# Kernel optimization log

Measured on AMD Instinct MI355X. Metric: run time of the kernel, lower is better.

## Reference

```python
import jax, jax.numpy as jnp
import numpy as np

FEAT = 2048
NUM_CLASSES = 751
EPS = 1e-5


def setup_inputs() -> dict:
    key = jax.random.key(0)
    k1, k2, k3 = jax.random.split(key, 3)
    probe_x = jax.random.normal(k1, (64, FEAT), dtype=jnp.float32)
    gallery_x = jax.random.normal(k2, (256, FEAT), dtype=jnp.float32)
    # BatchNorm1d affine params (PyTorch init: gamma=1, beta=0)
    bn_gamma = jnp.ones((FEAT,), dtype=jnp.float32)
    bn_beta = jnp.zeros((FEAT,), dtype=jnp.float32)
    # classifier: weight ~ N(0, 0.001), bias = 0
    W = jax.random.normal(k3, (NUM_CLASSES, FEAT), dtype=jnp.float32) * 0.001
    b = jnp.zeros((NUM_CLASSES,), dtype=jnp.float32)
    return {"probe_x": probe_x, "gallery_x": gallery_x,
            "bn_gamma": bn_gamma, "bn_beta": bn_beta, "W": W, "b": b}


def reference(probe_x, gallery_x, bn_gamma, bn_beta, W, b):
    n_probe, feat = probe_x.shape
    n_gallery = gallery_x.shape[0]
    # broadcast squared difference: [Np, Ng, F]
    diff = jnp.square(probe_x[:, None, :] - gallery_x[None, :, :])
    d = diff.reshape(n_probe * n_gallery, feat)
    # BatchNorm1d in training mode: biased batch statistics over the batch dim
    mean = jnp.mean(d, axis=0)
    var = jnp.mean(jnp.square(d - mean), axis=0)
    bn = (d - mean) * (bn_gamma / jnp.sqrt(var + EPS)) + bn_beta
    # Linear classifier
    cls = jnp.einsum('nf,cf->nc', bn, W) + b
    return cls.reshape(n_probe, n_gallery, -1)
```

## Files before the change

### kernel.cpp

```cpp
#include <hip/hip_runtime.h>
#include <hip/hip_bf16.h>
#include <hip/hip_fp16.h>

#define FEAT 2048
#define NCLS 751
#define NPAD 768
#define NPRB 64
#define NGAL 256
#define WSCALE 256.0f

typedef _Float16 f16x8 __attribute__((ext_vector_type(8)));
typedef float f32x4 __attribute__((ext_vector_type(4)));

__device__ __forceinline__ unsigned short f2h_u(float x) {
  union { _Float16 h; unsigned short u; } v;
  v.h = (_Float16)x;
  return v.u;
}

__global__ void stats_kernel(const float* __restrict__ P, const float* __restrict__ G,
                             const float* __restrict__ gamma, const float* __restrict__ beta,
                             float* __restrict__ st) {
  int fx = threadIdx.x & 31, ry = threadIdx.x >> 5;
  int f = blockIdx.x * 32 + fx;
  float a1 = 0, a2 = 0, a3 = 0, a4 = 0;
  for (int r = ry; r < NPRB; r += 8) {
    float x = P[r * FEAT + f], x2 = x * x;
    a1 += x; a2 += x2; a3 += x2 * x; a4 += x2 * x2;
  }
  float b1 = 0, b2 = 0, b3 = 0, b4 = 0;
  for (int r = ry; r < NGAL; r += 8) {
    float x = G[r * FEAT + f], x2 = x * x;
    b1 += x; b2 += x2; b3 += x2 * x; b4 += x2 * x2;
  }
  __shared__ float red[8][8][32];
  float vals[8] = {a1, a2, a3, a4, b1, b2, b3, b4};
#pragma unroll
  for (int m = 0; m < 8; ++m) red[m][ry][fx] = vals[m];
  __syncthreads();
  if (ry == 0) {
    float mm[8];
#pragma unroll
    for (int m = 0; m < 8; ++m) {
      float sum = 0.f;
#pragma unroll
      for (int r = 0; r < 8; ++r) sum += red[m][r][fx];
      mm[m] = sum;
    }
    float M1p = mm[0] * (1.f / NPRB), M2p = mm[1] * (1.f / NPRB);
    float M3p = mm[2] * (1.f / NPRB), M4p = mm[3] * (1.f / NPRB);
    float M1g = mm[4] * (1.f / NGAL), M2g = mm[5] * (1.f / NGAL);
    float M3g = mm[6] * (1.f / NGAL), M4g = mm[7] * (1.f / NGAL);
    float mean = M2p - 2.f * M1p * M1g + M2g;
    float Ed2 = M4p - 4.f * M3p * M1g + 6.f * M2p * M2g - 4.f * M1p * M3g + M4g;
    float var = Ed2 - mean * mean;
    float sv = gamma[f] / sqrtf(var + 1e-5f);
    st[f] = sv;
    st[FEAT + f] = beta[f] - mean * sv;
  }
}

__global__ void prepw_kernel(const float* __restrict__ W, const float* __restrict__ b,
                             const float* __restrict__ st,
                             unsigned short* __restrict__ Wp, float* __restrict__ bp) {
  int c = blockIdx.x;
  int f = threadIdx.x * 8;
  float4 w0 = make_float4(0.f, 0.f, 0.f, 0.f), w1 = w0;
  if (c < NCLS) {
    const float4* wsrc = (const float4*)(W + (size_t)c * FEAT + f);
    w0 = wsrc[0]; w1 = wsrc[1];
  }
  const float4* s4 = (const float4*)(st + f);
  float4 s0 = s4[0], s1 = s4[1];
  const float4* t4 = (const float4*)(st + FEAT + f);
  float4 t0 = t4[0], t1 = t4[1];
  uint4 u;
  u.x = (unsigned int)f2h_u(w0.x * s0.x * WSCALE) | ((unsigned int)f2h_u(w0.y * s0.y * WSCALE) << 16);
  u.y = (unsigned int)f2h_u(w0.z * s0.z * WSCALE) | ((unsigned int)f2h_u(w0.w * s0.w * WSCALE) << 16);
  u.z = (unsigned int)f2h_u(w1.x * s1.x * WSCALE) | ((unsigned int)f2h_u(w1.y * s1.y * WSCALE) << 16);
  u.w = (unsigned int)f2h_u(w1.z * s1.z * WSCALE) | ((unsigned int)f2h_u(w1.w * s1.w * WSCALE) << 16);
  *(uint4*)(Wp + (size_t)c * FEAT + f) = u;
  float acc = t0.x * w0.x + t0.y * w0.y + t0.z * w0.z + t0.w * w0.w +
              t1.x * w1.x + t1.y * w1.y + t1.z * w1.z + t1.w * w1.w;
#pragma unroll
  for (int off = 32; off > 0; off >>= 1) acc += __shfl_down(acc, off, 64);
  __shared__ float r[4];
  int wave = threadIdx.x >> 6, lane = threadIdx.x & 63;
  if (lane == 0) r[wave] = acc;
  __syncthreads();
  if (threadIdx.x == 0) bp[c] = (c < NCLS ? b[c] : 0.f) + r[0] + r[1] + r[2] + r[3];
}

__global__ void agen_kernel(const float* __restrict__ P, const float* __restrict__ G,
                            unsigned short* __restrict__ A) {
  int n = blockIdx.x;
  int p = n >> 8, g = n & 255;
  int f = threadIdx.x * 8;
  const float4* p4 = (const float4*)(P + (size_t)p * FEAT + f);
  const float4* g4 = (const float4*)(G + (size_t)g * FEAT + f);
  float4 pa = p4[0], pb = p4[1];
  float4 ga = g4[0], gb = g4[1];
  float d0 = pa.x - ga.x, d1 = pa.y - ga.y, d2 = pa.z - ga.z, d3 = pa.w - ga.w;
  float d4 = pb.x - gb.x, d5 = pb.y - gb.y, d6 = pb.z - gb.z, d7 = pb.w - gb.w;
  uint4 u;
  u.x = (unsigned int)f2h_u(d0 * d0) | ((unsigned int)f2h_u(d1 * d1) << 16);
  u.y = (unsigned int)f2h_u(d2 * d2) | ((unsigned int)f2h_u(d3 * d3) << 16);
  u.z = (unsigned int)f2h_u(d4 * d4) | ((unsigned int)f2h_u(d5 * d5) << 16);
  u.w = (unsigned int)f2h_u(d6 * d6) | ((unsigned int)f2h_u(d7 * d7) << 16);
  *(uint4*)(A + (size_t)n * FEAT + f) = u;
}

__global__ __launch_bounds__(256, 3)
void gemm_mat_kernel(const unsigned short* __restrict__ A,
                     const unsigned short* __restrict__ Wp,
                     const float* __restrict__ bp, float* __restrict__ out) {
  __shared__ unsigned short As[128 * 64];
  __shared__ unsigned short Bs[128 * 64];

  const int tid = threadIdx.x;
  const int lane = tid & 63, wave = tid >> 6;
  const int mtile = blockIdx.x, ntile = blockIdx.y;

  const int srow = tid >> 3;
  const int sch = (tid & 7) ^ (srow & 7);
  const unsigned short* ag = A + (size_t)(mtile * 128 + srow) * FEAT + sch * 8;
  const unsigned short* bg = Wp + (size_t)(ntile * 128 + srow) * FEAT + sch * 8;
  char* alds = (char*)As + wave * 1024;
  char* blds = (char*)Bs + wave * 1024;

  f32x4 acc[4][4];
#pragma unroll
  for (int mi = 0; mi < 4; ++mi)
#pragma unroll
    for (int ni = 0; ni < 4; ++ni) acc[mi][ni] = (f32x4){0.f, 0.f, 0.f, 0.f};

  const int wm = (wave & 1) * 64, wn = (wave >> 1) * 64;
  const int frow = lane & 15, fsw = lane & 7, fk = lane >> 4;

  for (int k0 = 0; k0 < FEAT; k0 += 64) {
    __syncthreads();
#pragma unroll
    for (int j = 0; j < 4; ++j) {
      __builtin_amdgcn_global_load_lds(
          (const __attribute__((address_space(1))) void*)(ag + k0 + (size_t)j * 32 * FEAT),
          (__attribute__((address_space(3))) void*)(alds + j * 4096), 16, 0, 0);
      __builtin_amdgcn_global_load_lds(
          (const __attribute__((address_space(1))) void*)(bg + k0 + (size_t)j * 32 * FEAT),
          (__attribute__((address_space(3))) void*)(blds + j * 4096), 16, 0, 0);
    }
    __syncthreads();

#pragma unroll
    for (int kk = 0; kk < 2; ++kk) {
      const int slot = (kk * 4 + fk) ^ fsw;
      f16x8 af[4], bf[4];
#pragma unroll
      for (int mi = 0; mi < 4; ++mi)
        af[mi] = *(const f16x8*)(As + (wm + mi * 16 + frow) * 64 + slot * 8);
#pragma unroll
      for (int ni = 0; ni < 4; ++ni)
        bf[ni] = *(const f16x8*)(Bs + (wn + ni * 16 + frow) * 64 + slot * 8);
#pragma unroll
      for (int mi = 0; mi < 4; ++mi)
#pragma unroll
        for (int ni = 0; ni < 4; ++ni)
          acc[mi][ni] = __builtin_amdgcn_mfma_f32_16x16x32_f16(af[mi], bf[ni], acc[mi][ni], 0, 0, 0);
    }
  }

  const int col0 = ntile * 128 + wn + (lane & 15);
  const int row0 = mtile * 128 + wm + ((lane >> 4) << 2);
#pragma unroll
  for (int ni = 0; ni < 4; ++ni) {
    int col = col0 + ni * 16;
    if (col >= NCLS) continue;
    float bv = bp[col];
#pragma unroll
    for (int mi = 0; mi < 4; ++mi) {
      int row = row0 + mi * 16;
#pragma unroll
      for (int r = 0; r < 4; ++r)
        out[(size_t)(row + r) * NCLS + col] = acc[mi][ni][r] * (1.0f / WSCALE) + bv;
    }
  }
}

extern "C" void kernel_launch(void* const* d_in, const int* in_sizes, int n_in,
                              void* d_out, int out_size, void* d_ws, size_t ws_size,
                              hipStream_t stream) {
  const float* P = (const float*)d_in[0];
  const float* G = (const float*)d_in[1];
  const float* gamma = (const float*)d_in[2];
  const float* beta = (const float*)d_in[3];
  const float* W = (const float*)d_in[4];
  const float* b = (const float*)d_in[5];
  float* out = (float*)d_out;

  float* st = (float*)d_ws;
  float* bp = st + 2 * FEAT;
  unsigned short* Wp = (unsigned short*)(bp + NPAD);
  unsigned short* A = Wp + (size_t)NPAD * FEAT;

  hipLaunchKernelGGL(agen_kernel, dim3(NPRB * NGAL), dim3(256), 0, stream, P, G, A);
  hipLaunchKernelGGL(stats_kernel, dim3(64), dim3(256), 0, stream, P, G, gamma, beta, st);
  hipLaunchKernelGGL(prepw_kernel, dim3(NPAD), dim3(256), 0, stream, W, b, st, Wp, bp);
  hipLaunchKernelGGL(gemm_mat_kernel, dim3(128, 6), dim3(256), 0, stream, A, Wp, bp, out);
}
```

Before: 166.8 us.

## Pre-swizzle weights into MFMA fragment layout and load B directly to registers

The weight-prep kernel now writes the scaled fp16 weights in a fragment-ordered layout, so each GEMM lane can read its B operand straight from global memory into registers with one coalesced vector load. This removes the B shared-memory tile and its LDS reads, and the B loads for the next k-step are double-buffered in registers while the current one computes. The cost is more registers, which could affect occupancy under launch_bounds(256,3). The prep kernel also drops from 768 blocks to 48 blocks, each looping over the whole feature dimension.

```diff
diff --git a/kernel.cpp b/kernel.cpp
--- a/kernel.cpp
+++ b/kernel.cpp
@@ -62,33 +62,45 @@
 
 __global__ void prepw_kernel(const float* __restrict__ W, const float* __restrict__ b,
                              const float* __restrict__ st,
-                             unsigned short* __restrict__ Wp, float* __restrict__ bp) {
-  int c = blockIdx.x;
-  int f = threadIdx.x * 8;
-  float4 w0 = make_float4(0.f, 0.f, 0.f, 0.f), w1 = w0;
-  if (c < NCLS) {
-    const float4* wsrc = (const float4*)(W + (size_t)c * FEAT + f);
-    w0 = wsrc[0]; w1 = wsrc[1];
-  }
-  const float4* s4 = (const float4*)(st + f);
-  float4 s0 = s4[0], s1 = s4[1];
-  const float4* t4 = (const float4*)(st + FEAT + f);
-  float4 t0 = t4[0], t1 = t4[1];
-  uint4 u;
-  u.x = (unsigned int)f2h_u(w0.x * s0.x * WSCALE) | ((unsigned int)f2h_u(w0.y * s0.y * WSCALE) << 16);
-  u.y = (unsigned int)f2h_u(w0.z * s0.z * WSCALE) | ((unsigned int)f2h_u(w0.w * s0.w * WSCALE) << 16);
-  u.z = (unsigned int)f2h_u(w1.x * s1.x * WSCALE) | ((unsigned int)f2h_u(w1.y * s1.y * WSCALE) << 16);
-  u.w = (unsigned int)f2h_u(w1.z * s1.z * WSCALE) | ((unsigned int)f2h_u(w1.w * s1.w * WSCALE) << 16);
-  *(uint4*)(Wp + (size_t)c * FEAT + f) = u;
-  float acc = t0.x * w0.x + t0.y * w0.y + t0.z * w0.z + t0.w * w0.w +
-              t1.x * w1.x + t1.y * w1.y + t1.z * w1.z + t1.w * w1.w;
-#pragma unroll
-  for (int off = 32; off > 0; off >>= 1) acc += __shfl_down(acc, off, 64);
-  __shared__ float r[4];
-  int wave = threadIdx.x >> 6, lane = threadIdx.x & 63;
-  if (lane == 0) r[wave] = acc;
+                             unsigned short* __restrict__ Wf, float* __restrict__ bp) {
+  const int nblk = blockIdx.x;
+  const int t = threadIdx.x;
+  const int row = t & 15;
+  const int c = nblk * 16 + row;
+  const int kcb = t >> 4;
+  unsigned short* wbase = Wf + (size_t)nblk * 32768;
+  float part = 0.f;
+#pragma unroll 4
+  for (int i = 0; i < 16; ++i) {
+    int kc = i * 16 + kcb;
+    int f = kc * 8;
+    float4 w0 = make_float4(0.f, 0.f, 0.f, 0.f), w1 = w0;
+    if (c < NCLS) {
+      const float4* ws = (const float4*)(W + (size_t)c * FEAT + f);
+      w0 = ws[0]; w1 = ws[1];
+    }
+    const float4* s4 = (const float4*)(st + f);
+    float4 s0 = s4[0], s1 = s4[1];
+    const float4* t4 = (const float4*)(st + FEAT + f);
+    float4 t0 = t4[0], t1 = t4[1];
+    uint4 u;
+    u.x = (unsigned int)f2h_u(w0.x * s0.x * WSCALE) | ((unsigned int)f2h_u(w0.y * s0.y * WSCALE) << 16);
+    u.y = (unsigned int)f2h_u(w0.z * s0.z * WSCALE) | ((unsigned int)f2h_u(w0.w * s0.w * WSCALE) << 16);
+    u.z = (unsigned int)f2h_u(w1.x * s1.x * WSCALE) | ((unsigned int)f2h_u(w1.y * s1.y * WSCALE) << 16);
+    u.w = (unsigned int)f2h_u(w1.z * s1.z * WSCALE) | ((unsigned int)f2h_u(w1.w * s1.w * WSCALE) << 16);
+    *(uint4*)(wbase + (size_t)kc * 128 + row * 8) = u;
+    part += t0.x * w0.x + t0.y * w0.y + t0.z * w0.z + t0.w * w0.w +
+            t1.x * w1.x + t1.y * w1.y + t1.z * w1.z + t1.w * w1.w;
+  }
+  __shared__ float red[16][16];
+  red[kcb][row] = part;
   __syncthreads();
-  if (threadIdx.x == 0) bp[c] = (c < NCLS ? b[c] : 0.f) + r[0] + r[1] + r[2] + r[3];
+  if (t < 16) {
+    float sum = (nblk * 16 + t < NCLS) ? b[nblk * 16 + t] : 0.f;
+#pragma unroll
+    for (int j = 0; j < 16; ++j) sum += red[j][t];
+    bp[nblk * 16 + t] = sum;
+  }
 }
 
 __global__ void agen_kernel(const float* __restrict__ P, const float* __restrict__ G,
@@ -112,10 +124,9 @@
 
 __global__ __launch_bounds__(256, 3)
 void gemm_mat_kernel(const unsigned short* __restrict__ A,
-                     const unsigned short* __restrict__ Wp,
+                     const unsigned short* __restrict__ Wf,
                      const float* __restrict__ bp, float* __restrict__ out) {
   __shared__ unsigned short As[128 * 64];
-  __shared__ unsigned short Bs[128 * 64];
 
   const int tid = threadIdx.x;
   const int lane = tid & 63, wave = tid >> 6;
@@ -124,9 +135,7 @@
   const int srow = tid >> 3;
   const int sch = (tid & 7) ^ (srow & 7);
   const unsigned short* ag = A + (size_t)(mtile * 128 + srow) * FEAT + sch * 8;
-  const unsigned short* bg = Wp + (size_t)(ntile * 128 + srow) * FEAT + sch * 8;
   char* alds = (char*)As + wave * 1024;
-  char* blds = (char*)Bs + wave * 1024;
 
   f32x4 acc[4][4];
 #pragma unroll
@@ -137,36 +146,53 @@
   const int wm = (wave & 1) * 64, wn = (wave >> 1) * 64;
   const int frow = lane & 15, fsw = lane & 7, fk = lane >> 4;
 
-  for (int k0 = 0; k0 < FEAT; k0 += 64) {
-    __syncthreads();
-#pragma unroll
-    for (int j = 0; j < 4; ++j) {
-      __builtin_amdgcn_global_load_lds(
-          (const __attribute__((address_space(1))) void*)(ag + k0 + (size_t)j * 32 * FEAT),
-          (__attribute__((address_space(3))) void*)(alds + j * 4096), 16, 0, 0);
-      __builtin_amdgcn_global_load_lds(
-          (const __attribute__((address_space(1))) void*)(bg + k0 + (size_t)j * 32 * FEAT),
-          (__attribute__((address_space(3))) void*)(blds + j * 4096), 16, 0, 0);
-    }
-    __syncthreads();
-
-#pragma unroll
-    for (int kk = 0; kk < 2; ++kk) {
-      const int slot = (kk * 4 + fk) ^ fsw;
-      f16x8 af[4], bf[4];
-#pragma unroll
-      for (int mi = 0; mi < 4; ++mi)
-        af[mi] = *(const f16x8*)(As + (wm + mi * 16 + frow) * 64 + slot * 8);
-#pragma unroll
-      for (int ni = 0; ni < 4; ++ni)
-        bf[ni] = *(const f16x8*)(Bs + (wn + ni * 16 + frow) * 64 + slot * 8);
-#pragma unroll
-      for (int mi = 0; mi < 4; ++mi)
-#pragma unroll
-        for (int ni = 0; ni < 4; ++ni)
-          acc[mi][ni] = __builtin_amdgcn_mfma_f32_16x16x32_f16(af[mi], bf[ni], acc[mi][ni], 0, 0, 0);
-    }
-  }
+  const unsigned short* wfbase =
+      Wf + ((size_t)ntile * 8 + (wn >> 4)) * 32768 + lane * 8;
+
+  f16x8 bfa[2][4], bfb[2][4];
+#pragma unroll
+  for (int kk = 0; kk < 2; ++kk)
+#pragma unroll
+    for (int ni = 0; ni < 4; ++ni)
+      bfa[kk][ni] = *(const f16x8*)(wfbase + (size_t)ni * 32768 + kk * 512);
+
+#define STAGE_A(K0)                                                              \
+  do {                                                                           \
+    __syncthreads();                                                             \
+    _Pragma("unroll") for (int j = 0; j < 4; ++j)                                \
+        __builtin_amdgcn_global_load_lds(                                        \
+            (const __attribute__((address_space(1))) void*)(ag + (K0) +          \
+                                                            (size_t)j * 32 * FEAT), \
+            (__attribute__((address_space(3))) void*)(alds + j * 4096), 16, 0, 0);
+#define PREFETCH_B(DST, K0)                                                      \
+    _Pragma("unroll") for (int kk = 0; kk < 2; ++kk)                             \
+      _Pragma("unroll") for (int ni = 0; ni < 4; ++ni)                           \
+        DST[kk][ni] = *(const f16x8*)(wfbase + (size_t)ni * 32768 + (K0)*16 + kk * 512);
+#define COMPUTE(SRC)                                                             \
+    __syncthreads();                                                             \
+    _Pragma("unroll") for (int kk = 0; kk < 2; ++kk) {                           \
+      const int slot = (kk * 4 + fk) ^ fsw;                                      \
+      f16x8 af[4];                                                               \
+      _Pragma("unroll") for (int mi = 0; mi < 4; ++mi)                           \
+          af[mi] = *(const f16x8*)(As + (wm + mi * 16 + frow) * 64 + slot * 8);  \
+      _Pragma("unroll") for (int mi = 0; mi < 4; ++mi)                           \
+        _Pragma("unroll") for (int ni = 0; ni < 4; ++ni)                         \
+            acc[mi][ni] = __builtin_amdgcn_mfma_f32_16x16x32_f16(                \
+                af[mi], SRC[kk][ni], acc[mi][ni], 0, 0, 0);                      \
+    }                                                                            \
+  } while (0)
+
+  for (int k0 = 0; k0 < FEAT; k0 += 128) {
+    STAGE_A(k0)
+    PREFETCH_B(bfb, k0 + 64)
+    COMPUTE(bfa);
+    STAGE_A(k0 + 64)
+    if (k0 + 128 < FEAT) { PREFETCH_B(bfa, k0 + 128) }
+    COMPUTE(bfb);
+  }
+#undef STAGE_A
+#undef PREFETCH_B
+#undef COMPUTE
 
   const int col0 = ntile * 128 + wn + (lane & 15);
   const int row0 = mtile * 128 + wm + ((lane >> 4) << 2);
@@ -198,11 +224,11 @@
 
   float* st = (float*)d_ws;
   float* bp = st + 2 * FEAT;
-  unsigned short* Wp = (unsigned short*)(bp + NPAD);
-  unsigned short* A = Wp + (size_t)NPAD * FEAT;
+  unsigned short* Wf = (unsigned short*)(bp + NPAD);
+  unsigned short* A = Wf + (size_t)48 * 32768;
 
   hipLaunchKernelGGL(agen_kernel, dim3(NPRB * NGAL), dim3(256), 0, stream, P, G, A);
   hipLaunchKernelGGL(stats_kernel, dim3(64), dim3(256), 0, stream, P, G, gamma, beta, st);
-  hipLaunchKernelGGL(prepw_kernel, dim3(NPAD), dim3(256), 0, stream, W, b, st, Wp, bp);
-  hipLaunchKernelGGL(gemm_mat_kernel, dim3(128, 6), dim3(256), 0, stream, A, Wp, bp, out);
-}
+  hipLaunchKernelGGL(prepw_kernel, dim3(48), dim3(256), 0, stream, W, b, st, Wf, bp);
+  hipLaunchKernelGGL(gemm_mat_kernel, dim3(128, 6), dim3(256), 0, stream, A, Wf, bp, out);
+}
```

Measured after the change: 190.6 us. 1.14x slower.

## Merge stats and weight prep into agen kernels to cut launches

Applied to the files above, without the earlier changes.

Merges the four-kernel pipeline into three launches. The stats computation runs alongside the first half of the A-matrix generation in one kernel, and the weight prep runs alongside the second half in another. Weight prep is restructured so each block handles 16 classes with a loop over features, using 48 blocks instead of 768. The intent is to remove launch gaps and overlap the small serial stats and prep stages with the bandwidth-bound A generation, at the cost of giving the prep work much less parallelism.

```diff
diff --git a/kernel.cpp b/kernel.cpp
--- a/kernel.cpp
+++ b/kernel.cpp
@@ -18,84 +18,12 @@
   return v.u;
 }
 
-__global__ void stats_kernel(const float* __restrict__ P, const float* __restrict__ G,
-                             const float* __restrict__ gamma, const float* __restrict__ beta,
-                             float* __restrict__ st) {
-  int fx = threadIdx.x & 31, ry = threadIdx.x >> 5;
-  int f = blockIdx.x * 32 + fx;
-  float a1 = 0, a2 = 0, a3 = 0, a4 = 0;
-  for (int r = ry; r < NPRB; r += 8) {
-    float x = P[r * FEAT + f], x2 = x * x;
-    a1 += x; a2 += x2; a3 += x2 * x; a4 += x2 * x2;
-  }
-  float b1 = 0, b2 = 0, b3 = 0, b4 = 0;
-  for (int r = ry; r < NGAL; r += 8) {
-    float x = G[r * FEAT + f], x2 = x * x;
-    b1 += x; b2 += x2; b3 += x2 * x; b4 += x2 * x2;
-  }
-  __shared__ float red[8][8][32];
-  float vals[8] = {a1, a2, a3, a4, b1, b2, b3, b4};
-#pragma unroll
-  for (int m = 0; m < 8; ++m) red[m][ry][fx] = vals[m];
-  __syncthreads();
-  if (ry == 0) {
-    float mm[8];
-#pragma unroll
-    for (int m = 0; m < 8; ++m) {
-      float sum = 0.f;
-#pragma unroll
-      for (int r = 0; r < 8; ++r) sum += red[m][r][fx];
-      mm[m] = sum;
-    }
-    float M1p = mm[0] * (1.f / NPRB), M2p = mm[1] * (1.f / NPRB);
-    float M3p = mm[2] * (1.f / NPRB), M4p = mm[3] * (1.f / NPRB);
-    float M1g = mm[4] * (1.f / NGAL), M2g = mm[5] * (1.f / NGAL);
-    float M3g = mm[6] * (1.f / NGAL), M4g = mm[7] * (1.f / NGAL);
-    float mean = M2p - 2.f * M1p * M1g + M2g;
-    float Ed2 = M4p - 4.f * M3p * M1g + 6.f * M2p * M2g - 4.f * M1p * M3g + M4g;
-    float var = Ed2 - mean * mean;
-    float sv = gamma[f] / sqrtf(var + 1e-5f);
-    st[f] = sv;
-    st[FEAT + f] = beta[f] - mean * sv;
-  }
-}
-
-__global__ void prepw_kernel(const float* __restrict__ W, const float* __restrict__ b,
-                             const float* __restrict__ st,
-                             unsigned short* __restrict__ Wp, float* __restrict__ bp) {
-  int c = blockIdx.x;
-  int f = threadIdx.x * 8;
-  float4 w0 = make_float4(0.f, 0.f, 0.f, 0.f), w1 = w0;
-  if (c < NCLS) {
-    const float4* wsrc = (const float4*)(W + (size_t)c * FEAT + f);
-    w0 = wsrc[0]; w1 = wsrc[1];
-  }
-  const float4* s4 = (const float4*)(st + f);
-  float4 s0 = s4[0], s1 = s4[1];
-  const float4* t4 = (const float4*)(st + FEAT + f);
-  float4 t0 = t4[0], t1 = t4[1];
-  uint4 u;
-  u.x = (unsigned int)f2h_u(w0.x * s0.x * WSCALE) | ((unsigned int)f2h_u(w0.y * s0.y * WSCALE) << 16);
-  u.y = (unsigned int)f2h_u(w0.z * s0.z * WSCALE) | ((unsigned int)f2h_u(w0.w * s0.w * WSCALE) << 16);
-  u.z = (unsigned int)f2h_u(w1.x * s1.x * WSCALE) | ((unsigned int)f2h_u(w1.y * s1.y * WSCALE) << 16);
-  u.w = (unsigned int)f2h_u(w1.z * s1.z * WSCALE) | ((unsigned int)f2h_u(w1.w * s1.w * WSCALE) << 16);
-  *(uint4*)(Wp + (size_t)c * FEAT + f) = u;
-  float acc = t0.x * w0.x + t0.y * w0.y + t0.z * w0.z + t0.w * w0.w +
-              t1.x * w1.x + t1.y * w1.y + t1.z * w1.z + t1.w * w1.w;
-#pragma unroll
-  for (int off = 32; off > 0; off >>= 1) acc += __shfl_down(acc, off, 64);
-  __shared__ float r[4];
-  int wave = threadIdx.x >> 6, lane = threadIdx.x & 63;
-  if (lane == 0) r[wave] = acc;
-  __syncthreads();
-  if (threadIdx.x == 0) bp[c] = (c < NCLS ? b[c] : 0.f) + r[0] + r[1] + r[2] + r[3];
-}
-
-__global__ void agen_kernel(const float* __restrict__ P, const float* __restrict__ G,
-                            unsigned short* __restrict__ A) {
-  int n = blockIdx.x;
+__device__ __forceinline__ void agen_row(const float* __restrict__ P,
+                                         const float* __restrict__ G,
+                                         unsigned short* __restrict__ A,
+                                         int n, int tid) {
   int p = n >> 8, g = n & 255;
-  int f = threadIdx.x * 8;
+  int f = tid * 8;
   const float4* p4 = (const float4*)(P + (size_t)p * FEAT + f);
   const float4* g4 = (const float4*)(G + (size_t)g * FEAT + f);
   float4 pa = p4[0], pb = p4[1];
@@ -110,10 +38,105 @@
   *(uint4*)(A + (size_t)n * FEAT + f) = u;
 }
 
+__global__ void k1_stats_agen(const float* __restrict__ P, const float* __restrict__ G,
+                              const float* __restrict__ gamma, const float* __restrict__ beta,
+                              float* __restrict__ st, unsigned short* __restrict__ A) {
+  const int blk = blockIdx.x, tid = threadIdx.x;
+  if (blk < 64) {
+    __shared__ float red[8][8][32];
+    int fx = tid & 31, ry = tid >> 5;
+    int f = blk * 32 + fx;
+    float a1 = 0, a2 = 0, a3 = 0, a4 = 0;
+    for (int r = ry; r < NPRB; r += 8) {
+      float x = P[r * FEAT + f], x2 = x * x;
+      a1 += x; a2 += x2; a3 += x2 * x; a4 += x2 * x2;
+    }
+    float b1 = 0, b2 = 0, b3 = 0, b4 = 0;
+    for (int r = ry; r < NGAL; r += 8) {
+      float x = G[r * FEAT + f], x2 = x * x;
+      b1 += x; b2 += x2; b3 += x2 * x; b4 += x2 * x2;
+    }
+    float vals[8] = {a1, a2, a3, a4, b1, b2, b3, b4};
+#pragma unroll
+    for (int m = 0; m < 8; ++m) red[m][ry][fx] = vals[m];
+    __syncthreads();
+    if (ry == 0) {
+      float mm[8];
+#pragma unroll
+      for (int m = 0; m < 8; ++m) {
+        float sum = 0.f;
+#pragma unroll
+        for (int r = 0; r < 8; ++r) sum += red[m][r][fx];
+        mm[m] = sum;
+      }
+      float M1p = mm[0] * (1.f / NPRB), M2p = mm[1] * (1.f / NPRB);
+      float M3p = mm[2] * (1.f / NPRB), M4p = mm[3] * (1.f / NPRB);
+      float M1g = mm[4] * (1.f / NGAL), M2g = mm[5] * (1.f / NGAL);
+      float M3g = mm[6] * (1.f / NGAL), M4g = mm[7] * (1.f / NGAL);
+      float mean = M2p - 2.f * M1p * M1g + M2g;
+      float Ed2 = M4p - 4.f * M3p * M1g + 6.f * M2p * M2g - 4.f * M1p * M3g + M4g;
+      float var = Ed2 - mean * mean;
+      float sv = gamma[f] / sqrtf(var + 1e-5f);
+      st[f] = sv;
+      st[FEAT + f] = beta[f] - mean * sv;
+    }
+  } else {
+    for (int n = blk - 64; n < 8192; n += 512) agen_row(P, G, A, n, tid);
+  }
+}
+
+__global__ void k2_prepw_agen(const float* __restrict__ P, const float* __restrict__ G,
+                              const float* __restrict__ W, const float* __restrict__ b,
+                              const float* __restrict__ st,
+                              unsigned short* __restrict__ Wp, float* __restrict__ bp,
+                              unsigned short* __restrict__ A) {
+  const int blk = blockIdx.x, t = threadIdx.x;
+  if (blk < 48) {
+    const int nblk = blk;
+    const int row = t & 15;
+    const int c = nblk * 16 + row;
+    const int kcb = t >> 4;
+    float part = 0.f;
+#pragma unroll 4
+    for (int i = 0; i < 16; ++i) {
+      int kc = i * 16 + kcb;
+      int f = kc * 8;
+      float4 w0 = make_float4(0.f, 0.f, 0.f, 0.f), w1 = w0;
+      if (c < NCLS) {
+        const float4* ws = (const float4*)(W + (size_t)c * FEAT + f);
+        w0 = ws[0]; w1 = ws[1];
+      }
+      const float4* s4 = (const float4*)(st + f);
+      float4 s0 = s4[0], s1 = s4[1];
+      const float4* t4 = (const float4*)(st + FEAT + f);
+      float4 t0 = t4[0], t1 = t4[1];
+      uint4 u;
+      u.x = (unsigned int)f2h_u(w0.x * s0.x * WSCALE) | ((unsigned int)f2h_u(w0.y * s0.y * WSCALE) << 16);
+      u.y = (unsigned int)f2h_u(w0.z * s0.z * WSCALE) | ((unsigned int)f2h_u(w0.w * s0.w * WSCALE) << 16);
+      u.z = (unsigned int)f2h_u(w1.x * s1.x * WSCALE) | ((unsigned int)f2h_u(w1.y * s1.y * WSCALE) << 16);
+      u.w = (unsigned int)f2h_u(w1.z * s1.z * WSCALE) | ((unsigned int)f2h_u(w1.w * s1.w * WSCALE) << 16);
+      *(uint4*)(Wp + (size_t)c * FEAT + f) = u;
+      part += t0.x * w0.x + t0.y * w0.y + t0.z * w0.z + t0.w * w0.w +
+              t1.x * w1.x + t1.y * w1.y + t1.z * w1.z + t1.w * w1.w;
+    }
+    __shared__ float red[16][16];
+    red[kcb][row] = part;
+    __syncthreads();
+    if (t < 16) {
+      float sum = (nblk * 16 + t < NCLS) ? b[nblk * 16 + t] : 0.f;
+#pragma unroll
+      for (int j = 0; j < 16; ++j) sum += red[j][t];
+      bp[nblk * 16 + t] = sum;
+    }
+  } else {
+    for (int n = 8192 + (blk - 48); n < NPRB * NGAL; n += 512) agen_row(P, G, A, n, t);
+  }
+}
+
 __global__ __launch_bounds__(256, 3)
-void gemm_mat_kernel(const unsigned short* __restrict__ A,
-                     const unsigned short* __restrict__ Wp,
-                     const float* __restrict__ bp, float* __restrict__ out) {
+void gemm_kernel(const unsigned short* __restrict__ A,
+                 const unsigned short* __restrict__ Wp,
+                 const float* __restrict__ bp, float* __restrict__ out) {
   __shared__ unsigned short As[128 * 64];
   __shared__ unsigned short Bs[128 * 64];
 
@@ -201,8 +224,7 @@
   unsigned short* Wp = (unsigned short*)(bp + NPAD);
   unsigned short* A = Wp + (size_t)NPAD * FEAT;
 
-  hipLaunchKernelGGL(agen_kernel, dim3(NPRB * NGAL), dim3(256), 0, stream, P, G, A);
-  hipLaunchKernelGGL(stats_kernel, dim3(64), dim3(256), 0, stream, P, G, gamma, beta, st);
-  hipLaunchKernelGGL(prepw_kernel, dim3(NPAD), dim3(256), 0, stream, W, b, st, Wp, bp);
-  hipLaunchKernelGGL(gemm_mat_kernel, dim3(128, 6), dim3(256), 0, stream, A, Wp, bp, out);
-}
+  hipLaunchKernelGGL(k1_stats_agen, dim3(576), dim3(256), 0, stream, P, G, gamma, beta, st, A);
+  hipLaunchKernelGGL(k2_prepw_agen, dim3(560), dim3(256), 0, stream, P, G, W, b, st, Wp, bp, A);
+  hipLaunchKernelGGL(gemm_kernel, dim3(128, 6), dim3(256), 0, stream, A, Wp, bp, out);
+}
```

Measured after the change: 176.9 us. +6.0%, slower.
